# Optimization experiments

Hardware: AMD Instinct MI355X
Metric: run time of the kernel (lower is better)

The kernel has to match this reference:

```python
import jax, jax.numpy as jnp
import numpy as np
from jax import lax

B, S, H, W = 2, 512, 96, 120
NB, NH, D, DH = 4, 8, 256, 32
FLAT = 16 * 12 * 15  # 2880


def _conv(x, w, b):
    # x: [N, Cin, H, W], w: [Cout, Cin, 4, 4], stride 2, pad 1
    y = lax.conv_general_dilated(x, w, window_strides=(2, 2),
                                 padding=[(1, 1), (1, 1)],
                                 dimension_numbers=('NCHW', 'OIHW', 'NCHW'))
    return jax.nn.relu(y + b[None, :, None, None])


def _layernorm(x, g, b, eps=1e-5):
    mu = x.mean(axis=-1, keepdims=True)
    var = ((x - mu) ** 2).mean(axis=-1, keepdims=True)
    return (x - mu) * lax.rsqrt(var + eps) * g + b


def setup_inputs() -> dict:
    key = jax.random.key(0)
    ks = jax.random.split(key, 16)
    sc = 0.02
    return {
        'state': jax.random.normal(ks[0], (B, S, 3, H, W), jnp.float32),
        'conv_w1': jax.random.normal(ks[1], (16, 3, 4, 4), jnp.float32) * 0.1,
        'conv_b1': jnp.zeros((16,), jnp.float32),
        'conv_w2': jax.random.normal(ks[2], (16, 16, 4, 4), jnp.float32) * 0.1,
        'conv_b2': jnp.zeros((16,), jnp.float32),
        'conv_w3': jax.random.normal(ks[3], (16, 16, 4, 4), jnp.float32) * 0.1,
        'conv_b3': jnp.zeros((16,), jnp.float32),
        'pre_w': jax.random.normal(ks[4], (FLAT, D), jnp.float32) * sc,
        'pre_b': jnp.zeros((D,), jnp.float32),
        'pos_w': jax.random.normal(ks[5], (1, S, D), jnp.float32) * sc,
        'ln1_g': jnp.ones((NB, D), jnp.float32),
        'ln1_b': jnp.zeros((NB, D), jnp.float32),
        'enc_w': jax.random.normal(ks[6], (NB, D, 3 * D), jnp.float32) * sc,
        'enc_b': jnp.zeros((NB, 3 * D), jnp.float32),
        'ln2_g': jnp.ones((NB, D), jnp.float32),
        'ln2_b': jnp.zeros((NB, D), jnp.float32),
        'ffn_w1': jax.random.normal(ks[7], (NB, D, 4 * D), jnp.float32) * sc,
        'ffn_b1': jnp.zeros((NB, 4 * D), jnp.float32),
        'ffn_w2': jax.random.normal(ks[8], (NB, 4 * D, D), jnp.float32) * sc,
        'ffn_b2': jnp.zeros((NB, D), jnp.float32),
        'emb_w': jax.random.normal(ks[9], (D, D), jnp.float32) * sc,
        'emb_b': jnp.zeros((D,), jnp.float32),
    }


def reference(state, conv_w1, conv_b1, conv_w2, conv_b2, conv_w3, conv_b3,
              pre_w, pre_b, pos_w, ln1_g, ln1_b, enc_w, enc_b,
              ln2_g, ln2_b, ffn_w1, ffn_b1, ffn_w2, ffn_b2, emb_w, emb_b):
    b, s = state.shape[:2]
    x = state.reshape(b * s, 3, H, W)
    x = _conv(x, conv_w1, conv_b1)
    x = _conv(x, conv_w2, conv_b2)
    x = _conv(x, conv_w3, conv_b3)
    x = x.reshape(b, s, FLAT)
    x = x @ pre_w + pre_b          # [b,s,D]
    x = x + pos_w                  # positional embedding

    # causal mask, additive form as in original: w*m - 1e10*(1-m)
    i = jnp.arange(s)[:, None]
    j = jnp.arange(s)[None, :]
    m = (i >= j).astype(jnp.float32)[None, None]  # [1,1,s,s]
    scale = 1.0 / jnp.sqrt(jnp.float32(DH))

    for k in range(NB):
        xn = _layernorm(x, ln1_g[k], ln1_b[k])
        c = xn @ enc_w[k] + enc_b[k]              # [b,s,3D]
        q, kk, v = jnp.split(c, 3, axis=2)
        q = q.reshape(b, s, NH, DH).transpose(0, 2, 1, 3)
        kk = kk.reshape(b, s, NH, DH).transpose(0, 2, 1, 3)
        v = v.reshape(b, s, NH, DH).transpose(0, 2, 1, 3)
        w = jnp.einsum('bhqd,bhkd->bhqk', q, kk) * scale
        w = w * m - 1e10 * (1.0 - m)
        a = jax.nn.softmax(w, axis=3) @ v          # [b,h,s,dh]
        a = a.transpose(0, 2, 1, 3).reshape(b, s, NH * DH)
        x = x + a
        x = _layernorm(x, ln2_g[k], ln2_b[k])
        mm = jax.nn.gelu(x @ ffn_w1[k] + ffn_b1[k], approximate=False)
        mm = mm @ ffn_w2[k] + ffn_b2[k]
        x = x + mm

    enc = x @ emb_w + emb_b
    # global standardization with torch-style unbiased std (ddof=1)
    enc = (enc - enc.mean()) / jnp.std(enc, ddof=1) + 1e-10
    return enc
```

## Files before the change

### kernel.cpp

```cpp
#include <hip/hip_runtime.h>
#include <hip/hip_bf16.h>
#include <math.h>


#define DMODEL 256
#define SEQ    512

typedef __attribute__((ext_vector_type(8))) short bf16x8;
typedef __attribute__((ext_vector_type(4))) float f32x4;

static __device__ __forceinline__ unsigned short f2bf(float v) {
  __hip_bfloat16 h = __float2bfloat16(v);
  return *reinterpret_cast<unsigned short*>(&h);
}
static __device__ __forceinline__ float bf2f(unsigned short u) {
  __hip_bfloat16 h;
  *reinterpret_cast<unsigned short*>(&h) = u;
  return __bfloat162float(h);
}
static __device__ __forceinline__ void split2(float v, unsigned short& h,
                                              unsigned short& l) {
  h = f2bf(v);
  l = f2bf(v - bf2f(h));
}

__global__ __launch_bounds__(256) void conv1_kernel(
    const float* __restrict__ in, const float* __restrict__ w,
    const float* __restrict__ bias, float* __restrict__ out) {
  __shared__ float wsm[768];
  int t = threadIdx.x;
  for (int i = t; i < 768; i += 256) wsm[i] = w[i];
  __syncthreads();
  int idx = blockIdx.x * 256 + t;
  int ox = idx % 60;
  int oy = (idx / 60) % 48;
  int n  = idx / (60 * 48);
  int iy0 = oy * 2 - 1, ix0 = ox * 2 - 1;
  float win[3][16];
  #pragma unroll
  for (int ic = 0; ic < 3; ic++) {
    #pragma unroll
    for (int ky = 0; ky < 4; ky++) {
      int iy = iy0 + ky;
      #pragma unroll
      for (int kx = 0; kx < 4; kx++) {
        int ix = ix0 + kx;
        bool ok = (iy >= 0) && (iy < 96) && (ix >= 0) && (ix < 120);
        win[ic][ky * 4 + kx] = ok ? in[((n * 3 + ic) * 96 + iy) * 120 + ix] : 0.f;
      }
    }
  }
  #pragma unroll
  for (int oc = 0; oc < 16; oc++) {
    float acc = bias[oc];
    const float* wp = &wsm[oc * 48];
    #pragma unroll
    for (int ic = 0; ic < 3; ic++)
      #pragma unroll
      for (int k = 0; k < 16; k++)
        acc = fmaf(win[ic][k], wp[ic * 16 + k], acc);
    out[((n * 16 + oc) * 48 + oy) * 60 + ox] = fmaxf(acc, 0.f);
  }
}

template <int IH, int IW, int OH, int OW>
__global__ __launch_bounds__(256) void conv16_kernel(
    const float* __restrict__ in, const float* __restrict__ w,
    const float* __restrict__ bias, float* __restrict__ out) {
  __shared__ float wsm[4096];
  int t = threadIdx.x;
  for (int i = t; i < 4096; i += 256) wsm[i] = w[i];
  __syncthreads();
  int idx = blockIdx.x * 256 + t;
  int ox = idx % OW;
  int oy = (idx / OW) % OH;
  int n  = idx / (OW * OH);
  int iy0 = oy * 2 - 1, ix0 = ox * 2 - 1;
  float acc[16];
  #pragma unroll
  for (int oc = 0; oc < 16; oc++) acc[oc] = bias[oc];
  for (int ic = 0; ic < 16; ic++) {
    float win[16];
    #pragma unroll
    for (int ky = 0; ky < 4; ky++) {
      int iy = iy0 + ky;
      #pragma unroll
      for (int kx = 0; kx < 4; kx++) {
        int ix = ix0 + kx;
        bool ok = (iy >= 0) && (iy < IH) && (ix >= 0) && (ix < IW);
        win[ky * 4 + kx] = ok ? in[((n * 16 + ic) * IH + iy) * IW + ix] : 0.f;
      }
    }
    #pragma unroll
    for (int oc = 0; oc < 16; oc++) {
      const float* wp = &wsm[(oc * 16 + ic) * 16];
      float a = acc[oc];
      #pragma unroll
      for (int k = 0; k < 16; k++) a = fmaf(win[k], wp[k], a);
      acc[oc] = a;
    }
  }
  #pragma unroll
  for (int oc = 0; oc < 16; oc++)
    out[((n * 16 + oc) * OH + oy) * OW + ox] = fmaxf(acc[oc], 0.f);
}

__global__ __launch_bounds__(256) void tcvt_kernel(
    const float* __restrict__ W, unsigned short* __restrict__ Th,
    unsigned short* __restrict__ Tl, int K, int N) {
  __shared__ float lds[32][33];
  int t = threadIdx.x;
  int kt = blockIdx.x, nt = blockIdx.y, b = blockIdx.z;
  const float* Wb = W + (size_t)b * K * N;
  unsigned short* Thb = Th + (size_t)b * K * N;
  unsigned short* Tlb = Tl + (size_t)b * K * N;
  int c = t & 31, r0 = (t >> 5) * 4;
  #pragma unroll
  for (int i = 0; i < 4; i++)
    lds[r0 + i][c] = Wb[(size_t)(kt * 32 + r0 + i) * N + nt * 32 + c];
  __syncthreads();
  #pragma unroll
  for (int i = 0; i < 4; i++) {
    float v = lds[c][r0 + i];
    unsigned short h, l;
    split2(v, h, l);
    size_t o = (size_t)(nt * 32 + r0 + i) * K + kt * 32 + c;
    Thb[o] = h;
    Tlb[o] = l;
  }
}

__global__ __launch_bounds__(256) void cvtpair_kernel(
    const float4* __restrict__ in, unsigned short* __restrict__ oh,
    unsigned short* __restrict__ ol) {
  int i = blockIdx.x * 256 + threadIdx.x;
  float4 v = in[i];
  ushort4 H, L;
  split2(v.x, H.x, L.x);
  split2(v.y, H.y, L.y);
  split2(v.z, H.z, L.z);
  split2(v.w, H.w, L.w);
  *(ushort4*)&oh[i * 4] = H;
  *(ushort4*)&ol[i * 4] = L;
}

template <int EPI>
__global__ __launch_bounds__(256) void gemm_mfma_kernel(
    const unsigned short* __restrict__ Ah, const unsigned short* __restrict__ Al,
    const unsigned short* __restrict__ Bh, const unsigned short* __restrict__ Bl,
    const float* __restrict__ bias, float* __restrict__ C,
    unsigned short* __restrict__ Ch, unsigned short* __restrict__ Cl,
    int M, int N, int K, int klen) {
  __shared__ unsigned short As[2][128 * 40];
  __shared__ unsigned short Bs[2][128 * 40];
  int t = threadIdx.x;
  int n0 = blockIdx.x * 128, m0 = blockIdx.y * 128;
  int kb = blockIdx.z * klen;
  int w = t >> 6, l = t & 63;
  int wr = w >> 1, wc = w & 1;
  int fr = l & 15, fq = l >> 4;
  f32x4 acc[4][4];
  #pragma unroll
  for (int i = 0; i < 4; i++)
    #pragma unroll
    for (int j = 0; j < 4; j++) acc[i][j] = (f32x4){0.f, 0.f, 0.f, 0.f};

  for (int kt = 0; kt < klen; kt += 32) {
    int kg = kb + kt;
    #pragma unroll
    for (int s = 0; s < 2; s++) {
      int q = t + 256 * s;
      int row = q >> 2, ko = (q & 3) << 3;
      *(int4*)&As[0][row * 40 + ko] =
          *(const int4*)&Ah[(size_t)(m0 + row) * K + kg + ko];
      *(int4*)&As[1][row * 40 + ko] =
          *(const int4*)&Al[(size_t)(m0 + row) * K + kg + ko];
      *(int4*)&Bs[0][row * 40 + ko] =
          *(const int4*)&Bh[(size_t)(n0 + row) * K + kg + ko];
      *(int4*)&Bs[1][row * 40 + ko] =
          *(const int4*)&Bl[(size_t)(n0 + row) * K + kg + ko];
    }
    __syncthreads();
    bf16x8 ah[4], al4[4], bh4[4], bl4[4];
    #pragma unroll
    for (int fm = 0; fm < 4; fm++) {
      int ro = (wr * 64 + fm * 16 + fr) * 40 + fq * 8;
      ah[fm]  = *(const bf16x8*)&As[0][ro];
      al4[fm] = *(const bf16x8*)&As[1][ro];
    }
    #pragma unroll
    for (int fn = 0; fn < 4; fn++) {
      int ro = (wc * 64 + fn * 16 + fr) * 40 + fq * 8;
      bh4[fn] = *(const bf16x8*)&Bs[0][ro];
      bl4[fn] = *(const bf16x8*)&Bs[1][ro];
    }
    #pragma unroll
    for (int fm = 0; fm < 4; fm++)
      #pragma unroll
      for (int fn = 0; fn < 4; fn++) {
        acc[fm][fn] = __builtin_amdgcn_mfma_f32_16x16x32_bf16(
            ah[fm], bh4[fn], acc[fm][fn], 0, 0, 0);
        acc[fm][fn] = __builtin_amdgcn_mfma_f32_16x16x32_bf16(
            ah[fm], bl4[fn], acc[fm][fn], 0, 0, 0);
        acc[fm][fn] = __builtin_amdgcn_mfma_f32_16x16x32_bf16(
            al4[fm], bh4[fn], acc[fm][fn], 0, 0, 0);
      }
    __syncthreads();
  }

  #pragma unroll
  for (int fm = 0; fm < 4; fm++) {
    int rbase = m0 + wr * 64 + fm * 16 + fq * 4;
    #pragma unroll
    for (int fn = 0; fn < 4; fn++) {
      int col = n0 + wc * 64 + fn * 16 + fr;
      #pragma unroll
      for (int i = 0; i < 4; i++) {
        int m = rbase + i;
        float v = acc[fm][fn][i];
        if (EPI == 2) {
          atomicAdd(&C[(size_t)m * N + col], v);
        } else if (EPI == 0) {
          C[(size_t)m * N + col] = v + bias[col];
        } else {
          float g = v + bias[col];
          g = 0.5f * g * (1.f + erff(g * 0.70710678118654752f));
          unsigned short hh, ll;
          split2(g, hh, ll);
          Ch[(size_t)m * N + col] = hh;
          Cl[(size_t)m * N + col] = ll;
        }
      }
    }
  }
}

__global__ __launch_bounds__(256) void initpre4_kernel(
    float4* __restrict__ C, const float4* __restrict__ bias,
    const float4* __restrict__ pos) {
  int i = blockIdx.x * 256 + threadIdx.x;
  int n4 = i & 63;
  int m = i >> 6;
  float4 b = bias[n4], p = pos[(m & (SEQ - 1)) * 64 + n4];
  C[i] = make_float4(b.x + p.x, b.y + p.y, b.z + p.z, b.w + p.w);
}

__global__ __launch_bounds__(256) void addbias4_kernel(
    float4* __restrict__ C, const float4* __restrict__ bias) {
  int i = blockIdx.x * 256 + threadIdx.x;
  float4 v = C[i], b = bias[i & 63];
  v.x += b.x; v.y += b.y; v.z += b.z; v.w += b.w;
  C[i] = v;
}

__global__ __launch_bounds__(256) void ln1_bf_kernel(
    const float* __restrict__ x, const float* __restrict__ g,
    const float* __restrict__ b, unsigned short* __restrict__ oh,
    unsigned short* __restrict__ ol) {
  int lane = threadIdx.x & 63;
  int wid  = threadIdx.x >> 6;
  int row  = blockIdx.x * 4 + wid;
  const float* xr = x + row * DMODEL;
  float v[4];
  #pragma unroll
  for (int i = 0; i < 4; i++) v[i] = xr[lane + 64 * i];
  float s = v[0] + v[1] + v[2] + v[3];
  #pragma unroll
  for (int o = 32; o >= 1; o >>= 1) s += __shfl_xor(s, o);
  float mu = s * (1.f / 256.f);
  float sq = 0.f;
  #pragma unroll
  for (int i = 0; i < 4; i++) { float d = v[i] - mu; sq = fmaf(d, d, sq); }
  #pragma unroll
  for (int o = 32; o >= 1; o >>= 1) sq += __shfl_xor(sq, o);
  float rs = rsqrtf(sq * (1.f / 256.f) + 1e-5f);
  #pragma unroll
  for (int i = 0; i < 4; i++) {
    int c = lane + 64 * i;
    float vv = (v[i] - mu) * rs * g[c] + b[c];
    unsigned short h, l;
    split2(vv, h, l);
    oh[row * DMODEL + c] = h;
    ol[row * DMODEL + c] = l;
  }
}

__global__ __launch_bounds__(256) void ln2_bf_kernel(
    float* __restrict__ x, const float* __restrict__ g,
    const float* __restrict__ b, unsigned short* __restrict__ oh,
    unsigned short* __restrict__ ol) {
  int lane = threadIdx.x & 63;
  int wid  = threadIdx.x >> 6;
  int row  = blockIdx.x * 4 + wid;
  float* xr = x + row * DMODEL;
  float v[4];
  #pragma unroll
  for (int i = 0; i < 4; i++) v[i] = xr[lane + 64 * i];
  float s = v[0] + v[1] + v[2] + v[3];
  #pragma unroll
  for (int o = 32; o >= 1; o >>= 1) s += __shfl_xor(s, o);
  float mu = s * (1.f / 256.f);
  float sq = 0.f;
  #pragma unroll
  for (int i = 0; i < 4; i++) { float d = v[i] - mu; sq = fmaf(d, d, sq); }
  #pragma unroll
  for (int o = 32; o >= 1; o >>= 1) sq += __shfl_xor(sq, o);
  float rs = rsqrtf(sq * (1.f / 256.f) + 1e-5f);
  #pragma unroll
  for (int i = 0; i < 4; i++) {
    int c = lane + 64 * i;
    float vv = (v[i] - mu) * rs * g[c] + b[c];
    xr[c] = vv;
    unsigned short h, l;
    split2(vv, h, l);
    oh[row * DMODEL + c] = h;
    ol[row * DMODEL + c] = l;
  }
}

__global__ __launch_bounds__(256) void attn_fused_kernel(
    const float* __restrict__ qkv, float* __restrict__ x) {
  __shared__ float Qs[16][36];
  __shared__ float KVs[64][36];
  __shared__ float Osm[16][16][34];

  int t  = threadIdx.x;
  int it = blockIdx.x & 31;
  int h  = (blockIdx.x >> 5) & 7;
  int b  = blockIdx.x >> 8;
  int i0 = it * 16;
  int r  = t >> 4;
  int tx = t & 15;
  int i  = i0 + r;
  int njt = (it >> 2) + 1;

  if (t < 128) {
    int qrow = t >> 3, qd4 = t & 7;
    *(float4*)&Qs[qrow][qd4 * 4] =
        *(const float4*)&qkv[(b * SEQ + i0 + qrow) * 768 + h * 32 + qd4 * 4];
  }
  __syncthreads();
  float4 qv[8];
  #pragma unroll
  for (int d4 = 0; d4 < 8; d4++) qv[d4] = *(float4*)&Qs[r][d4 * 4];

  float s[32];
  #pragma unroll
  for (int z = 0; z < 32; z++) s[z] = -1e30f;

  int kr = t >> 2, kd4 = t & 3;

  #pragma unroll
  for (int jt = 0; jt < 8; jt++) {
    if (jt < njt) {
      int j0 = jt * 64;
      const float* kb = &qkv[(b * SEQ + j0 + kr) * 768 + DMODEL + h * 32];
      *(float4*)&KVs[kr][kd4 * 4]       = *(const float4*)&kb[kd4 * 4];
      *(float4*)&KVs[kr][(kd4 + 4) * 4] = *(const float4*)&kb[(kd4 + 4) * 4];
      __syncthreads();
      #pragma unroll
      for (int q = 0; q < 4; q++) {
        int jl = q * 16 + tx;
        int j  = j0 + jl;
        float acc = 0.f;
        #pragma unroll
        for (int d4 = 0; d4 < 8; d4++) {
          float4 kv = *(float4*)&KVs[jl][d4 * 4];
          acc = fmaf(qv[d4].x, kv.x, acc);
          acc = fmaf(qv[d4].y, kv.y, acc);
          acc = fmaf(qv[d4].z, kv.z, acc);
          acc = fmaf(qv[d4].w, kv.w, acc);
        }
        s[jt * 4 + q] = (j <= i) ? acc * 0.17677669529663687f : -1e30f;
      }
      __syncthreads();
    }
  }

  float mx = -1e30f;
  #pragma unroll
  for (int z = 0; z < 32; z++) mx = fmaxf(mx, s[z]);
  #pragma unroll
  for (int o = 8; o >= 1; o >>= 1) mx = fmaxf(mx, __shfl_xor(mx, o, 16));
  float sum = 0.f;
  #pragma unroll
  for (int z = 0; z < 32; z++) {
    float e = expf(s[z] - mx);
    s[z] = e;
    sum += e;
  }
  #pragma unroll
  for (int o = 8; o >= 1; o >>= 1) sum += __shfl_xor(sum, o, 16);
  float inv = 1.f / sum;
  #pragma unroll
  for (int z = 0; z < 32; z++) s[z] *= inv;

  float o[32];
  #pragma unroll
  for (int z = 0; z < 32; z++) o[z] = 0.f;

  #pragma unroll
  for (int jt = 0; jt < 8; jt++) {
    if (jt < njt) {
      int j0 = jt * 64;
      const float* vb = &qkv[(b * SEQ + j0 + kr) * 768 + 2 * DMODEL + h * 32];
      *(float4*)&KVs[kr][kd4 * 4]       = *(const float4*)&vb[kd4 * 4];
      *(float4*)&KVs[kr][(kd4 + 4) * 4] = *(const float4*)&vb[(kd4 + 4) * 4];
      __syncthreads();
      #pragma unroll
      for (int q = 0; q < 4; q++) {
        int jl = q * 16 + tx;
        float p = s[jt * 4 + q];
        #pragma unroll
        for (int d4 = 0; d4 < 8; d4++) {
          float4 vv = *(float4*)&KVs[jl][d4 * 4];
          o[d4 * 4 + 0] = fmaf(p, vv.x, o[d4 * 4 + 0]);
          o[d4 * 4 + 1] = fmaf(p, vv.y, o[d4 * 4 + 1]);
          o[d4 * 4 + 2] = fmaf(p, vv.z, o[d4 * 4 + 2]);
          o[d4 * 4 + 3] = fmaf(p, vv.w, o[d4 * 4 + 3]);
        }
      }
      __syncthreads();
    }
  }

  #pragma unroll
  for (int d2 = 0; d2 < 16; d2++)
    *(float2*)&Osm[r][tx][d2 * 2] = make_float2(o[d2 * 2], o[d2 * 2 + 1]);
  __syncthreads();
  float2 acc2 = make_float2(0.f, 0.f);
  #pragma unroll
  for (int tx2 = 0; tx2 < 16; tx2++) {
    float2 v = *(float2*)&Osm[r][tx2][tx * 2];
    acc2.x += v.x;
    acc2.y += v.y;
  }
  int base = (b * SEQ + i) * DMODEL + h * 32 + tx * 2;
  float2 old = *(float2*)&x[base];
  old.x += acc2.x;
  old.y += acc2.y;
  *(float2*)&x[base] = old;
}

__global__ __launch_bounds__(256) void reduce1_kernel(
    const float* __restrict__ enc, double* __restrict__ part) {
  int t = threadIdx.x;
  double s = 0.0, q = 0.0;
  for (int i = blockIdx.x * 256 + t; i < 262144; i += 256 * 256) {
    double v = (double)enc[i];
    s += v; q += v * v;
  }
  #pragma unroll
  for (int o = 32; o >= 1; o >>= 1) { s += __shfl_xor(s, o); q += __shfl_xor(q, o); }
  __shared__ double ls[4], lq[4];
  int lane = t & 63, wid = t >> 6;
  if (lane == 0) { ls[wid] = s; lq[wid] = q; }
  __syncthreads();
  if (t == 0) {
    part[blockIdx.x * 2]     = ls[0] + ls[1] + ls[2] + ls[3];
    part[blockIdx.x * 2 + 1] = lq[0] + lq[1] + lq[2] + lq[3];
  }
}

__global__ __launch_bounds__(256) void reduce2_kernel(
    const double* __restrict__ part, float* __restrict__ stats) {
  int t = threadIdx.x;
  double s = part[t * 2], q = part[t * 2 + 1];
  #pragma unroll
  for (int o = 32; o >= 1; o >>= 1) { s += __shfl_xor(s, o); q += __shfl_xor(q, o); }
  __shared__ double ls[4], lq[4];
  int lane = t & 63, wid = t >> 6;
  if (lane == 0) { ls[wid] = s; lq[wid] = q; }
  __syncthreads();
  if (t == 0) {
    double S = ls[0] + ls[1] + ls[2] + ls[3];
    double Q = lq[0] + lq[1] + lq[2] + lq[3];
    double n = 262144.0;
    double mean = S / n;
    double var  = (Q - n * mean * mean) / (n - 1.0);
    stats[0] = (float)mean;
    stats[1] = (float)(1.0 / sqrt(var));
  }
}

__global__ __launch_bounds__(256) void norm4_kernel(
    const float4* __restrict__ enc, const float* __restrict__ stats,
    float4* __restrict__ out) {
  int i = blockIdx.x * 256 + threadIdx.x;
  float mean = stats[0], inv = stats[1];
  float4 v = enc[i];
  v.x = (v.x - mean) * inv + 1e-10f;
  v.y = (v.y - mean) * inv + 1e-10f;
  v.z = (v.z - mean) * inv + 1e-10f;
  v.w = (v.w - mean) * inv + 1e-10f;
  out[i] = v;
}

extern "C" void kernel_launch(void* const* d_in, const int* in_sizes, int n_in,
                              void* d_out, int out_size, void* d_ws, size_t ws_size,
                              hipStream_t stream) {
  const float* state   = (const float*)d_in[0];
  const float* conv_w1 = (const float*)d_in[1];
  const float* conv_b1 = (const float*)d_in[2];
  const float* conv_w2 = (const float*)d_in[3];
  const float* conv_b2 = (const float*)d_in[4];
  const float* conv_w3 = (const float*)d_in[5];
  const float* conv_b3 = (const float*)d_in[6];
  const float* pre_w   = (const float*)d_in[7];
  const float* pre_b   = (const float*)d_in[8];
  const float* pos_w   = (const float*)d_in[9];
  const float* ln1_g   = (const float*)d_in[10];
  const float* ln1_b   = (const float*)d_in[11];
  const float* enc_w   = (const float*)d_in[12];
  const float* enc_bi  = (const float*)d_in[13];
  const float* ln2_g   = (const float*)d_in[14];
  const float* ln2_b   = (const float*)d_in[15];
  const float* ffn_w1  = (const float*)d_in[16];
  const float* ffn_b1  = (const float*)d_in[17];
  const float* ffn_w2  = (const float*)d_in[18];
  const float* ffn_b2  = (const float*)d_in[19];
  const float* emb_w   = (const float*)d_in[20];
  const float* emb_b   = (const float*)d_in[21];
  float* out = (float*)d_out;

  int nch = (ws_size >= (310ull << 20)) ? 1 : 4;
  int ipc = 1024 / nch;
  char* p = (char*)d_ws;
  auto alloc = [&](size_t bytes) {
    char* r = p;
    p += (bytes + 255) & ~(size_t)255;
    return r;
  };
  float* c1c = (float*)alloc((size_t)ipc * 46080 * 4);
  float* c2c = (float*)alloc((size_t)ipc * 11520 * 4);
  float* c3  = (float*)alloc(11796480);
  unsigned short* c3h  = (unsigned short*)alloc(5898240);
  unsigned short* c3l  = (unsigned short*)alloc(5898240);
  unsigned short* preTh = (unsigned short*)alloc(1474560);
  unsigned short* preTl = (unsigned short*)alloc(1474560);
  unsigned short* encTh = (unsigned short*)alloc(1572864);
  unsigned short* encTl = (unsigned short*)alloc(1572864);
  unsigned short* f1Th  = (unsigned short*)alloc(2097152);
  unsigned short* f1Tl  = (unsigned short*)alloc(2097152);
  unsigned short* f2Th  = (unsigned short*)alloc(2097152);
  unsigned short* f2Tl  = (unsigned short*)alloc(2097152);
  unsigned short* embTh = (unsigned short*)alloc(131072);
  unsigned short* embTl = (unsigned short*)alloc(131072);
  float* x    = (float*)alloc(1048576);
  unsigned short* xnh = (unsigned short*)alloc(524288);
  unsigned short* xnl = (unsigned short*)alloc(524288);
  unsigned short* xbh = (unsigned short*)alloc(524288);
  unsigned short* xbl = (unsigned short*)alloc(524288);
  float* qkv  = (float*)alloc(3145728);
  unsigned short* h1h = (unsigned short*)alloc(2097152);
  unsigned short* h1l = (unsigned short*)alloc(2097152);
  unsigned short* xfh = (unsigned short*)alloc(524288);
  unsigned short* xfl = (unsigned short*)alloc(524288);
  float* encb = (float*)alloc(1048576);
  double* part = (double*)alloc(4096);
  float* stats = (float*)alloc(256);

  tcvt_kernel<<<dim3(90, 8, 1), 256, 0, stream>>>(pre_w, preTh, preTl, 2880, 256);
  tcvt_kernel<<<dim3(8, 24, 4), 256, 0, stream>>>(enc_w, encTh, encTl, 256, 768);
  tcvt_kernel<<<dim3(8, 32, 4), 256, 0, stream>>>(ffn_w1, f1Th, f1Tl, 256, 1024);
  tcvt_kernel<<<dim3(32, 8, 4), 256, 0, stream>>>(ffn_w2, f2Th, f2Tl, 1024, 256);
  tcvt_kernel<<<dim3(8, 8, 1), 256, 0, stream>>>(emb_w, embTh, embTl, 256, 256);

  for (int ch = 0; ch < nch; ch++) {
    size_t so = (size_t)ch * ipc;
    conv1_kernel<<<ipc * 2880 / 256, 256, 0, stream>>>(
        state + so * 34560, conv_w1, conv_b1, c1c);
    conv16_kernel<48, 60, 24, 30><<<ipc * 720 / 256, 256, 0, stream>>>(
        c1c, conv_w2, conv_b2, c2c);
    conv16_kernel<24, 30, 12, 15><<<ipc * 180 / 256, 256, 0, stream>>>(
        c2c, conv_w3, conv_b3, c3 + so * 2880);
  }
  cvtpair_kernel<<<2880, 256, 0, stream>>>((const float4*)c3, c3h, c3l);

  initpre4_kernel<<<256, 256, 0, stream>>>(
      (float4*)x, (const float4*)pre_b, (const float4*)pos_w);
  gemm_mfma_kernel<2><<<dim3(2, 8, 5), 256, 0, stream>>>(
      c3h, c3l, preTh, preTl, nullptr, x, nullptr, nullptr,
      1024, 256, 2880, 576);

  for (int k = 0; k < 4; k++) {
    ln1_bf_kernel<<<256, 256, 0, stream>>>(x, ln1_g + k * 256, ln1_b + k * 256,
                                           xnh, xnl);
    gemm_mfma_kernel<0><<<dim3(6, 8, 1), 256, 0, stream>>>(
        xnh, xnl, encTh + (size_t)k * 196608, encTl + (size_t)k * 196608,
        enc_bi + k * 768, qkv, nullptr, nullptr, 1024, 768, 256, 256);
    attn_fused_kernel<<<512, 256, 0, stream>>>(qkv, x);
    ln2_bf_kernel<<<256, 256, 0, stream>>>(x, ln2_g + k * 256, ln2_b + k * 256,
                                           xbh, xbl);
    gemm_mfma_kernel<1><<<dim3(8, 8, 1), 256, 0, stream>>>(
        xbh, xbl, f1Th + (size_t)k * 262144, f1Tl + (size_t)k * 262144,
        ffn_b1 + k * 1024, nullptr, h1h, h1l, 1024, 1024, 256, 256);
    addbias4_kernel<<<256, 256, 0, stream>>>(
        (float4*)x, (const float4*)(ffn_b2 + k * 256));
    gemm_mfma_kernel<2><<<dim3(2, 8, 4), 256, 0, stream>>>(
        h1h, h1l, f2Th + (size_t)k * 262144, f2Tl + (size_t)k * 262144,
        nullptr, x, nullptr, nullptr, 1024, 256, 1024, 256);
  }

  cvtpair_kernel<<<256, 256, 0, stream>>>((const float4*)x, xfh, xfl);
  gemm_mfma_kernel<0><<<dim3(2, 8, 1), 256, 0, stream>>>(
      xfh, xfl, embTh, embTl, emb_b, encb, nullptr, nullptr,
      1024, 256, 256, 256);

  reduce1_kernel<<<256, 256, 0, stream>>>(encb, part);
  reduce2_kernel<<<1, 256, 0, stream>>>(part, stats);
  norm4_kernel<<<256, 256, 0, stream>>>((const float4*)encb, stats, (float4*)out);
}
```

Before: 1.003 ms.

## Stage conv input tiles in LDS and drop chunked conv launches

Rewrites the three conv layers so each block loads a zero-padded input band (or the whole image for conv3) into shared memory and reads the 4x4 windows from there as float2 pairs. This removes the per-tap bounds checks and the redundant, uncoalesced global loads of overlapping windows. Conv2 splits output channels across two thread halves, and threads beyond 240 or 180 sit idle after the load. The workspace-size chunking is removed and full-size intermediates are always allocated, which assumes the workspace is large enough.

```diff
diff --git a/kernel.cpp b/kernel.cpp
--- a/kernel.cpp
+++ b/kernel.cpp
@@ -24,72 +24,139 @@
   l = f2bf(v - bf2f(h));
 }
 
-__global__ __launch_bounds__(256) void conv1_kernel(
+__global__ __launch_bounds__(256) void conv1_lds_kernel(
     const float* __restrict__ in, const float* __restrict__ w,
     const float* __restrict__ bias, float* __restrict__ out) {
   __shared__ float wsm[768];
+  __shared__ float tin[3][10][124];
   int t = threadIdx.x;
+  int band = blockIdx.x % 12;
+  int n    = blockIdx.x / 12;
+  int oy0 = band * 4;
+  int gy0 = oy0 * 2 - 1;
   for (int i = t; i < 768; i += 256) wsm[i] = w[i];
-  __syncthreads();
-  int idx = blockIdx.x * 256 + t;
-  int ox = idx % 60;
-  int oy = (idx / 60) % 48;
-  int n  = idx / (60 * 48);
-  int iy0 = oy * 2 - 1, ix0 = ox * 2 - 1;
+  for (int idx = t; idx < 3 * 10 * 124; idx += 256) {
+    int c  = idx % 124;
+    int r  = (idx / 124) % 10;
+    int ic = idx / 1240;
+    int gy = gy0 + r, gx = c - 1;
+    float v = 0.f;
+    if (gx >= 0 && gx < 120 && gy >= 0 && gy < 96)
+      v = in[((n * 3 + ic) * 96 + gy) * 120 + gx];
+    tin[ic][r][c] = v;
+  }
+  __syncthreads();
+  if (t >= 240) return;
+  int ox = t % 60;
+  int ry = t / 60;
   float win[3][16];
   #pragma unroll
-  for (int ic = 0; ic < 3; ic++) {
-    #pragma unroll
-    for (int ky = 0; ky < 4; ky++) {
-      int iy = iy0 + ky;
-      #pragma unroll
-      for (int kx = 0; kx < 4; kx++) {
-        int ix = ix0 + kx;
-        bool ok = (iy >= 0) && (iy < 96) && (ix >= 0) && (ix < 120);
-        win[ic][ky * 4 + kx] = ok ? in[((n * 3 + ic) * 96 + iy) * 120 + ix] : 0.f;
-      }
-    }
-  }
+  for (int ic = 0; ic < 3; ic++)
+    #pragma unroll
+    for (int r = 0; r < 4; r++) {
+      float2 a = *(float2*)&tin[ic][ry * 2 + r][2 * ox];
+      float2 b = *(float2*)&tin[ic][ry * 2 + r][2 * ox + 2];
+      win[ic][r * 4 + 0] = a.x; win[ic][r * 4 + 1] = a.y;
+      win[ic][r * 4 + 2] = b.x; win[ic][r * 4 + 3] = b.y;
+    }
   #pragma unroll
   for (int oc = 0; oc < 16; oc++) {
     float acc = bias[oc];
-    const float* wp = &wsm[oc * 48];
-    #pragma unroll
-    for (int ic = 0; ic < 3; ic++)
+    #pragma unroll
+    for (int ic = 0; ic < 3; ic++) {
+      const float* wp = &wsm[oc * 48 + ic * 16];
       #pragma unroll
-      for (int k = 0; k < 16; k++)
-        acc = fmaf(win[ic][k], wp[ic * 16 + k], acc);
-    out[((n * 16 + oc) * 48 + oy) * 60 + ox] = fmaxf(acc, 0.f);
-  }
-}
-
-template <int IH, int IW, int OH, int OW>
-__global__ __launch_bounds__(256) void conv16_kernel(
+      for (int k = 0; k < 16; k++) acc = fmaf(win[ic][k], wp[k], acc);
+    }
+    out[((n * 16 + oc) * 48 + oy0 + ry) * 60 + ox] = fmaxf(acc, 0.f);
+  }
+}
+
+__global__ __launch_bounds__(256) void conv2_lds_kernel(
     const float* __restrict__ in, const float* __restrict__ w,
     const float* __restrict__ bias, float* __restrict__ out) {
   __shared__ float wsm[4096];
+  __shared__ float tin[16][10][64];
   int t = threadIdx.x;
+  int band = blockIdx.x % 6;
+  int n    = blockIdx.x / 6;
+  int oy0 = band * 4;
+  int gy0 = oy0 * 2 - 1;
   for (int i = t; i < 4096; i += 256) wsm[i] = w[i];
-  __syncthreads();
-  int idx = blockIdx.x * 256 + t;
-  int ox = idx % OW;
-  int oy = (idx / OW) % OH;
-  int n  = idx / (OW * OH);
-  int iy0 = oy * 2 - 1, ix0 = ox * 2 - 1;
-  float acc[16];
-  #pragma unroll
-  for (int oc = 0; oc < 16; oc++) acc[oc] = bias[oc];
+  for (int idx = t; idx < 16 * 10 * 64; idx += 256) {
+    int c  = idx & 63;
+    int r  = (idx >> 6) % 10;
+    int ic = idx / 640;
+    int gy = gy0 + r, gx = c - 1;
+    float v = 0.f;
+    if (gx >= 0 && gx < 60 && gy >= 0 && gy < 48)
+      v = in[((n * 16 + ic) * 48 + gy) * 60 + gx];
+    tin[ic][r][c] = v;
+  }
+  __syncthreads();
+  if (t >= 240) return;
+  int ox = t % 30;
+  int ry = (t / 30) % 4;
+  int oh = t / 120;
+  float acc[8];
+  #pragma unroll
+  for (int i = 0; i < 8; i++) acc[i] = bias[oh * 8 + i];
   for (int ic = 0; ic < 16; ic++) {
     float win[16];
     #pragma unroll
-    for (int ky = 0; ky < 4; ky++) {
-      int iy = iy0 + ky;
+    for (int r = 0; r < 4; r++) {
+      float2 a = *(float2*)&tin[ic][ry * 2 + r][2 * ox];
+      float2 b = *(float2*)&tin[ic][ry * 2 + r][2 * ox + 2];
+      win[r * 4 + 0] = a.x; win[r * 4 + 1] = a.y;
+      win[r * 4 + 2] = b.x; win[r * 4 + 3] = b.y;
+    }
+    #pragma unroll
+    for (int oc = 0; oc < 8; oc++) {
+      const float* wp = &wsm[((oh * 8 + oc) * 16 + ic) * 16];
+      float a = acc[oc];
       #pragma unroll
-      for (int kx = 0; kx < 4; kx++) {
-        int ix = ix0 + kx;
-        bool ok = (iy >= 0) && (iy < IH) && (ix >= 0) && (ix < IW);
-        win[ky * 4 + kx] = ok ? in[((n * 16 + ic) * IH + iy) * IW + ix] : 0.f;
-      }
+      for (int k = 0; k < 16; k++) a = fmaf(win[k], wp[k], a);
+      acc[oc] = a;
+    }
+  }
+  #pragma unroll
+  for (int oc = 0; oc < 8; oc++)
+    out[((n * 16 + oh * 8 + oc) * 24 + oy0 + ry) * 30 + ox] = fmaxf(acc[oc], 0.f);
+}
+
+__global__ __launch_bounds__(192) void conv3_lds_kernel(
+    const float* __restrict__ in, const float* __restrict__ w,
+    const float* __restrict__ bias, float* __restrict__ out) {
+  __shared__ float wsm[4096];
+  __shared__ float tin[16][26][32];
+  int t = threadIdx.x;
+  int n = blockIdx.x;
+  for (int i = t; i < 4096; i += 192) wsm[i] = w[i];
+  for (int idx = t; idx < 16 * 26 * 32; idx += 192) {
+    int c  = idx & 31;
+    int r  = (idx >> 5) % 26;
+    int ic = idx / 832;
+    int gy = r - 1, gx = c - 1;
+    float v = 0.f;
+    if (gx >= 0 && gx < 30 && gy >= 0 && gy < 24)
+      v = in[((n * 16 + ic) * 24 + gy) * 30 + gx];
+    tin[ic][r][c] = v;
+  }
+  __syncthreads();
+  if (t >= 180) return;
+  int ox = t % 15;
+  int oy = t / 15;
+  float acc[16];
+  #pragma unroll
+  for (int i = 0; i < 16; i++) acc[i] = bias[i];
+  for (int ic = 0; ic < 16; ic++) {
+    float win[16];
+    #pragma unroll
+    for (int r = 0; r < 4; r++) {
+      float2 a = *(float2*)&tin[ic][oy * 2 + r][2 * ox];
+      float2 b = *(float2*)&tin[ic][oy * 2 + r][2 * ox + 2];
+      win[r * 4 + 0] = a.x; win[r * 4 + 1] = a.y;
+      win[r * 4 + 2] = b.x; win[r * 4 + 3] = b.y;
     }
     #pragma unroll
     for (int oc = 0; oc < 16; oc++) {
@@ -102,7 +169,7 @@
   }
   #pragma unroll
   for (int oc = 0; oc < 16; oc++)
-    out[((n * 16 + oc) * OH + oy) * OW + ox] = fmaxf(acc[oc], 0.f);
+    out[((n * 16 + oc) * 12 + oy) * 15 + ox] = fmaxf(acc[oc], 0.f);
 }
 
 __global__ __launch_bounds__(256) void tcvt_kernel(
@@ -523,16 +590,14 @@
   const float* emb_b   = (const float*)d_in[21];
   float* out = (float*)d_out;
 
-  int nch = (ws_size >= (310ull << 20)) ? 1 : 4;
-  int ipc = 1024 / nch;
   char* p = (char*)d_ws;
   auto alloc = [&](size_t bytes) {
     char* r = p;
     p += (bytes + 255) & ~(size_t)255;
     return r;
   };
-  float* c1c = (float*)alloc((size_t)ipc * 46080 * 4);
-  float* c2c = (float*)alloc((size_t)ipc * 11520 * 4);
+  float* c1c = (float*)alloc((size_t)1024 * 46080 * 4);
+  float* c2c = (float*)alloc((size_t)1024 * 11520 * 4);
   float* c3  = (float*)alloc(11796480);
   unsigned short* c3h  = (unsigned short*)alloc(5898240);
   unsigned short* c3l  = (unsigned short*)alloc(5898240);
@@ -566,15 +631,9 @@
   tcvt_kernel<<<dim3(32, 8, 4), 256, 0, stream>>>(ffn_w2, f2Th, f2Tl, 1024, 256);
   tcvt_kernel<<<dim3(8, 8, 1), 256, 0, stream>>>(emb_w, embTh, embTl, 256, 256);
 
-  for (int ch = 0; ch < nch; ch++) {
-    size_t so = (size_t)ch * ipc;
-    conv1_kernel<<<ipc * 2880 / 256, 256, 0, stream>>>(
-        state + so * 34560, conv_w1, conv_b1, c1c);
-    conv16_kernel<48, 60, 24, 30><<<ipc * 720 / 256, 256, 0, stream>>>(
-        c1c, conv_w2, conv_b2, c2c);
-    conv16_kernel<24, 30, 12, 15><<<ipc * 180 / 256, 256, 0, stream>>>(
-        c2c, conv_w3, conv_b3, c3 + so * 2880);
-  }
+  conv1_lds_kernel<<<12288, 256, 0, stream>>>(state, conv_w1, conv_b1, c1c);
+  conv2_lds_kernel<<<6144, 256, 0, stream>>>(c1c, conv_w2, conv_b2, c2c);
+  conv3_lds_kernel<<<1024, 192, 0, stream>>>(c2c, conv_w3, conv_b3, c3);
   cvtpair_kernel<<<2880, 256, 0, stream>>>((const float4*)c3, c3h, c3l);
 
   initpre4_kernel<<<256, 256, 0, stream>>>(
```

New measurement: 1.302 ms. 29.8% more time.
